# Optimization experiments

Hardware: AMD Instinct MI355X
Metric: run time of the kernel (lower is better)

Reference implementation:

```python
import jax, jax.numpy as jnp
import numpy as np

BN_EPS = 1e-5

def _bn_train(h, gamma, beta):
    # BatchNorm1d in training mode: biased batch stats over the edge (batch) dim
    mean = jnp.mean(h, axis=0)
    var = jnp.var(h, axis=0)
    return (h - mean) * jax.lax.rsqrt(var + BN_EPS) * gamma + beta

def setup_inputs() -> dict:
    key = jax.random.key(0)
    ks = jax.random.split(key, 8)
    N, C, E = 50000, 128, 600000
    x = jax.random.normal(ks[0], (N, C), dtype=jnp.float32)
    edge_index = jax.random.randint(ks[1], (2, E), 0, N, dtype=jnp.int64)
    # Linear params, Kaiming-uniform-ish scale (values don't matter for correctness)
    def lin(k, fan_in, fan_out):
        k1, k2 = jax.random.split(k)
        bound = 1.0 / np.sqrt(fan_in)
        W = jax.random.uniform(k1, (fan_out, fan_in), jnp.float32, -bound, bound)
        b = jax.random.uniform(k2, (fan_out,), jnp.float32, -bound, bound)
        return W, b
    W1, b1 = lin(ks[2], 2 * C, C)
    W2, b2 = lin(ks[3], C, C)
    W3, b3 = lin(ks[4], C, 1)
    g1 = jnp.ones((C,), jnp.float32); be1 = jnp.zeros((C,), jnp.float32)
    g2 = jnp.ones((C,), jnp.float32); be2 = jnp.zeros((C,), jnp.float32)
    return {"x": x, "edge_index": edge_index,
            "W1": W1, "b1": b1, "g1": g1, "be1": be1,
            "W2": W2, "b2": b2, "g2": g2, "be2": be2,
            "W3": W3, "b3": b3}

def reference(x, edge_index, W1, b1, g1, be1, W2, b2, g2, be2, W3, b3):
    # gather endpoint features and concat: [E, 2C]
    ef = jnp.concatenate([x[edge_index[0]], x[edge_index[1]]], axis=1)
    h = jnp.einsum('ec,oc->eo', ef, W1) + b1          # [E, C]
    h = jax.nn.relu(_bn_train(h, g1, be1))
    h = jnp.einsum('ec,oc->eo', h, W2) + b2           # [E, C]
    h = jax.nn.relu(_bn_train(h, g2, be2))
    h = jnp.einsum('ec,oc->eo', h, W3) + b3           # [E, 1]
    return jnp.squeeze(h)                             # [E]
```

## Files before the change

### kernel.cpp

```cpp
#include <hip/hip_runtime.h>
#include <hip/hip_bf16.h>

#define CH 128

constexpr float BN_EPS = 1e-5f;

typedef short bf16x8 __attribute__((ext_vector_type(8)));
typedef float f32x4  __attribute__((ext_vector_type(4)));

__device__ __forceinline__ unsigned cvtpk_bf16(float lo, float hi) {
    unsigned r;
    asm("v_cvt_pk_bf16_f32 %0, %1, %2" : "=v"(r) : "v"(lo), "v"(hi));
    return r;
}
__device__ __forceinline__ float bf2f_lo(unsigned u) { return __uint_as_float(u << 16); }
__device__ __forceinline__ float bf2f_hi(unsigned u) { return __uint_as_float(u & 0xffff0000u); }

__device__ __forceinline__ void lds_barrier() {
    asm volatile("s_waitcnt lgkmcnt(0)\n\ts_barrier" ::: "memory");
}

union BF8 { bf16x8 v; unsigned u[4]; };

__device__ __forceinline__ bf16x8 pack8(float f0, float f1, float f2, float f3,
                                        float f4, float f5, float f6, float f7) {
    BF8 r;
    r.u[0] = cvtpk_bf16(f0, f1);
    r.u[1] = cvtpk_bf16(f2, f3);
    r.u[2] = cvtpk_bf16(f4, f5);
    r.u[3] = cvtpk_bf16(f6, f7);
    return r.v;
}

__global__ __launch_bounds__(512, 4) void node_linear_kernel(
    const float* __restrict__ x, const float* __restrict__ W1,
    unsigned short* __restrict__ u_bf, unsigned short* __restrict__ v_bf, int N)
{
    __shared__ short xs[64 * 128];

    const int t = threadIdx.x;
    const int lane = t & 63;
    const int wv = t >> 6;
    const int l15 = lane & 15;
    const int l4 = lane >> 4;
    const int n0 = blockIdx.x * 64;

    bf16x8 wfrag[2][4];
    #pragma unroll
    for (int ot = 0; ot < 2; ++ot) {
        const int o_ = wv * 32 + ot * 16 + l15;
        const float* wrow = (o_ < 128) ? (W1 + (size_t)o_ * 256)
                                       : (W1 + (size_t)(o_ - 128) * 256 + 128);
        #pragma unroll
        for (int kk = 0; kk < 4; ++kk) {
            float4 a = *(const float4*)(wrow + kk * 32 + l4 * 8);
            float4 b = *(const float4*)(wrow + kk * 32 + l4 * 8 + 4);
            wfrag[ot][kk] = pack8(a.x, a.y, a.z, a.w, b.x, b.y, b.z, b.w);
        }
    }

    const int c16 = t & 15;
    const int cb = c16 * 8;
    const int nsl = t >> 4;
    #pragma unroll
    for (int nn = 0; nn < 2; ++nn) {
        const int n_loc = nsl + nn * 32;
        const int n = n0 + n_loc;
        bf16x8 xv = {0, 0, 0, 0, 0, 0, 0, 0};
        if (n < N) {
            float4 a = *(const float4*)(x + (size_t)n * CH + cb);
            float4 b = *(const float4*)(x + (size_t)n * CH + cb + 4);
            xv = pack8(a.x, a.y, a.z, a.w, b.x, b.y, b.z, b.w);
        }
        *(bf16x8*)(xs + n_loc * 128 + (c16 ^ (n_loc & 7)) * 8) = xv;
    }
    __syncthreads();

    unsigned short* ob = (wv < 4) ? u_bf : v_bf;
    const int chb = (wv & 3) * 32;

    #pragma unroll
    for (int g = 0; g < 4; ++g) {
        const int nrow = g * 16 + l15;
        f32x4 D0 = {0.f, 0.f, 0.f, 0.f};
        f32x4 D1 = {0.f, 0.f, 0.f, 0.f};
        #pragma unroll
        for (int kk = 0; kk < 4; ++kk) {
            bf16x8 a = *(const bf16x8*)(xs + nrow * 128 + ((kk * 4 + l4) ^ (l15 & 7)) * 8);
            D0 = __builtin_amdgcn_mfma_f32_16x16x32_bf16(a, wfrag[0][kk], D0, 0, 0, 0);
            D1 = __builtin_amdgcn_mfma_f32_16x16x32_bf16(a, wfrag[1][kk], D1, 0, 0, 0);
        }
        #pragma unroll
        for (int r = 0; r < 4; ++r) {
            const int n = n0 + g * 16 + l4 * 4 + r;
            if (n < N) {
                unsigned pk = cvtpk_bf16(D0[r], D1[r]);
                ob[(size_t)n * CH + chb + l15]      = (unsigned short)pk;
                ob[(size_t)n * CH + chb + 16 + l15] = (unsigned short)(pk >> 16);
            }
        }
    }
}

__global__ __launch_bounds__(256) void stats1_kernel(
    const unsigned short* __restrict__ u_bf, const unsigned short* __restrict__ v_bf,
    const int* __restrict__ src, const int* __restrict__ dst,
    float* __restrict__ partials, int E)
{
    const int t = threadIdx.x;
    const int c8 = t & 31;
    const int eslot = t >> 5;
    const uint2* u2 = (const uint2*)u_bf;
    const uint2* v2 = (const uint2*)v_bf;

    float rs0=0.f, rs1=0.f, rs2=0.f, rs3=0.f;
    float rq0=0.f, rq1=0.f, rq2=0.f, rq3=0.f;

    const int iters = (E + 15) >> 4;
    for (int it = blockIdx.x; it < iters; it += gridDim.x) {
        const int e0 = it * 16 + eslot;
        const int e1 = e0 + 8;
        if (e0 < E) {
            const int s = src[e0], d = dst[e0];
            const uint2 a = u2[(size_t)s * 32 + c8];
            const uint2 b = v2[(size_t)d * 32 + c8];
            float h;
            h = bf2f_lo(a.x) + bf2f_lo(b.x); rs0 += h; rq0 += h * h;
            h = bf2f_hi(a.x) + bf2f_hi(b.x); rs1 += h; rq1 += h * h;
            h = bf2f_lo(a.y) + bf2f_lo(b.y); rs2 += h; rq2 += h * h;
            h = bf2f_hi(a.y) + bf2f_hi(b.y); rs3 += h; rq3 += h * h;
        }
        if (e1 < E) {
            const int s = src[e1], d = dst[e1];
            const uint2 a = u2[(size_t)s * 32 + c8];
            const uint2 b = v2[(size_t)d * 32 + c8];
            float h;
            h = bf2f_lo(a.x) + bf2f_lo(b.x); rs0 += h; rq0 += h * h;
            h = bf2f_hi(a.x) + bf2f_hi(b.x); rs1 += h; rq1 += h * h;
            h = bf2f_lo(a.y) + bf2f_lo(b.y); rs2 += h; rq2 += h * h;
            h = bf2f_hi(a.y) + bf2f_hi(b.y); rs3 += h; rq3 += h * h;
        }
    }
    __shared__ float red[256];
    red[t] = 0.f;
    __syncthreads();
    const int c = c8 * 4;
    atomicAdd(&red[c + 0], rs0); atomicAdd(&red[c + 1], rs1);
    atomicAdd(&red[c + 2], rs2); atomicAdd(&red[c + 3], rs3);
    atomicAdd(&red[128 + c + 0], rq0); atomicAdd(&red[128 + c + 1], rq1);
    atomicAdd(&red[128 + c + 2], rq2); atomicAdd(&red[128 + c + 3], rq3);
    __syncthreads();
    partials[(size_t)blockIdx.x * 256 + t] = red[t];
}

__global__ __launch_bounds__(1024) void finalize_kernel(
    const float* __restrict__ partials, int nblocks,
    const float* __restrict__ gamma, const float* __restrict__ beta,
    const float* __restrict__ bias,
    float* __restrict__ scale, float* __restrict__ shift, float invE)
{
    __shared__ float accs[1024], accq[1024];
    const int t = threadIdx.x;
    const int ch = t & 127;
    const int sl = t >> 7;
    float s = 0.f, q = 0.f;
    for (int b = sl; b < nblocks; b += 8) {
        s += partials[(size_t)b * 256 + ch];
        q += partials[(size_t)b * 256 + 128 + ch];
    }
    accs[t] = s; accq[t] = q;
    __syncthreads();
    if (t < 128) {
        float st = 0.f, qt = 0.f;
        #pragma unroll
        for (int k = 0; k < 8; ++k) { st += accs[k * 128 + t]; qt += accq[k * 128 + t]; }
        const float m0 = st * invE;
        const float var = fmaxf(qt * invE - m0 * m0, 0.f);
        const float mean = m0 + (bias ? bias[t] : 0.f);
        const float sc = gamma[t] * rsqrtf(var + BN_EPS);
        scale[t] = sc;
        shift[t] = beta[t] - mean * sc;
    }
}

__global__ __launch_bounds__(512, 4) void layer2_kernel(
    const unsigned short* __restrict__ u_bf, const unsigned short* __restrict__ v_bf,
    const int* __restrict__ src, const int* __restrict__ dst,
    const float* __restrict__ b1,
    const float* __restrict__ scale1, const float* __restrict__ shift1,
    const float* __restrict__ W2, const float* __restrict__ b2,
    uint2* __restrict__ h2raw, float* __restrict__ partials, int E)
{
    __shared__ short ybuf[2][64 * 128];
    __shared__ float red[256];

    const int t = threadIdx.x;
    const int lane = t & 63;
    const int wv = t >> 6;
    const int p = wv & 3;
    const int h = wv >> 2;
    const int l15 = lane & 15;
    const int l4  = lane >> 4;

    bf16x8 wfrag[2][4];
    #pragma unroll
    for (int ot = 0; ot < 2; ++ot) {
        const int o = p * 32 + ot * 16 + l15;
        #pragma unroll
        for (int kk = 0; kk < 4; ++kk) {
            const float* wp = W2 + (size_t)o * CH + kk * 32 + l4 * 8;
            float4 a = *(const float4*)wp;
            float4 bq = *(const float4*)(wp + 4);
            wfrag[ot][kk] = pack8(a.x, a.y, a.z, a.w, bq.x, bq.y, bq.z, bq.w);
        }
    }
    float b2r[2][4];
    #pragma unroll
    for (int ot = 0; ot < 2; ++ot)
        #pragma unroll
        for (int r = 0; r < 4; ++r)
            b2r[ot][r] = b2[p * 32 + ot * 16 + l4 * 4 + r];

    const int c16 = t & 15;
    const int cb = c16 * 8;
    const int ebase = t >> 4;
    const float4 sca = *(const float4*)(scale1 + cb);
    const float4 scb = *(const float4*)(scale1 + cb + 4);
    const float4 sha = *(const float4*)(shift1 + cb);
    const float4 shb = *(const float4*)(shift1 + cb + 4);
    const float4 b1a = *(const float4*)(b1 + cb);
    const float4 b1b = *(const float4*)(b1 + cb + 4);
    float4 bsa, bsb;
    bsa.x = b1a.x*sca.x + sha.x; bsa.y = b1a.y*sca.y + sha.y;
    bsa.z = b1a.z*sca.z + sha.z; bsa.w = b1a.w*sca.w + sha.w;
    bsb.x = b1b.x*scb.x + shb.x; bsb.y = b1b.y*scb.y + shb.y;
    bsb.z = b1b.z*scb.z + shb.z; bsb.w = b1b.w*scb.w + shb.w;

    float rs[2][4] = {{0.f,0.f,0.f,0.f},{0.f,0.f,0.f,0.f}};
    float rq[2][4] = {{0.f,0.f,0.f,0.f},{0.f,0.f,0.f,0.f}};

    const int ntiles = (E + 63) >> 6;
    const int tstep = gridDim.x;

    uint4 ua0, va0, ua1, va1;
    int tile = blockIdx.x;
    if (tile < ntiles) {
        const int eA = tile * 64 + ebase;
        const int eB = eA + 32;
        const int cA = eA < E ? eA : E - 1;
        const int cB = eB < E ? eB : E - 1;
        const int sA = src[cA], dA = dst[cA];
        const int sB = src[cB], dB = dst[cB];
        ua0 = *(const uint4*)(u_bf + (size_t)sA * CH + cb);
        va0 = *(const uint4*)(v_bf + (size_t)dA * CH + cb);
        ua1 = *(const uint4*)(u_bf + (size_t)sB * CH + cb);
        va1 = *(const uint4*)(v_bf + (size_t)dB * CH + cb);
    }

    int cur = 0;
    for (; tile < ntiles; tile += tstep) {
        {
            const int e = tile * 64 + ebase;
            bf16x8 y8 = {0, 0, 0, 0, 0, 0, 0, 0};
            if (e < E) {
                const float f0 = bf2f_lo(ua0.x) + bf2f_lo(va0.x);
                const float f1 = bf2f_hi(ua0.x) + bf2f_hi(va0.x);
                const float f2 = bf2f_lo(ua0.y) + bf2f_lo(va0.y);
                const float f3 = bf2f_hi(ua0.y) + bf2f_hi(va0.y);
                const float f4 = bf2f_lo(ua0.z) + bf2f_lo(va0.z);
                const float f5 = bf2f_hi(ua0.z) + bf2f_hi(va0.z);
                const float f6 = bf2f_lo(ua0.w) + bf2f_lo(va0.w);
                const float f7 = bf2f_hi(ua0.w) + bf2f_hi(va0.w);
                y8 = pack8(fmaxf(f0 * sca.x + bsa.x, 0.f),
                           fmaxf(f1 * sca.y + bsa.y, 0.f),
                           fmaxf(f2 * sca.z + bsa.z, 0.f),
                           fmaxf(f3 * sca.w + bsa.w, 0.f),
                           fmaxf(f4 * scb.x + bsb.x, 0.f),
                           fmaxf(f5 * scb.y + bsb.y, 0.f),
                           fmaxf(f6 * scb.z + bsb.z, 0.f),
                           fmaxf(f7 * scb.w + bsb.w, 0.f));
            }
            *(bf16x8*)(ybuf[cur] + ebase * 128 + (c16 ^ (ebase & 7)) * 8) = y8;
        }
        {
            const int e_loc = ebase + 32;
            const int e = tile * 64 + e_loc;
            bf16x8 y8 = {0, 0, 0, 0, 0, 0, 0, 0};
            if (e < E) {
                const float f0 = bf2f_lo(ua1.x) + bf2f_lo(va1.x);
                const float f1 = bf2f_hi(ua1.x) + bf2f_hi(va1.x);
                const float f2 = bf2f_lo(ua1.y) + bf2f_lo(va1.y);
                const float f3 = bf2f_hi(ua1.y) + bf2f_hi(va1.y);
                const float f4 = bf2f_lo(ua1.z) + bf2f_lo(va1.z);
                const float f5 = bf2f_hi(ua1.z) + bf2f_hi(va1.z);
                const float f6 = bf2f_lo(ua1.w) + bf2f_lo(va1.w);
                const float f7 = bf2f_hi(ua1.w) + bf2f_hi(va1.w);
                y8 = pack8(fmaxf(f0 * sca.x + bsa.x, 0.f),
                           fmaxf(f1 * sca.y + bsa.y, 0.f),
                           fmaxf(f2 * sca.z + bsa.z, 0.f),
                           fmaxf(f3 * sca.w + bsa.w, 0.f),
                           fmaxf(f4 * scb.x + bsb.x, 0.f),
                           fmaxf(f5 * scb.y + bsb.y, 0.f),
                           fmaxf(f6 * scb.z + bsb.z, 0.f),
                           fmaxf(f7 * scb.w + bsb.w, 0.f));
            }
            *(bf16x8*)(ybuf[cur] + e_loc * 128 + (c16 ^ (ebase & 7)) * 8) = y8;
        }

        const int ntile = tile + tstep;
        if (ntile < ntiles) {
            const int eA = ntile * 64 + ebase;
            const int eB = eA + 32;
            const int cA = eA < E ? eA : E - 1;
            const int cB = eB < E ? eB : E - 1;
            const int sA = src[cA], dA = dst[cA];
            const int sB = src[cB], dB = dst[cB];
            ua0 = *(const uint4*)(u_bf + (size_t)sA * CH + cb);
            va0 = *(const uint4*)(v_bf + (size_t)dA * CH + cb);
            ua1 = *(const uint4*)(u_bf + (size_t)sB * CH + cb);
            va1 = *(const uint4*)(v_bf + (size_t)dB * CH + cb);
        }

        lds_barrier();

        #pragma unroll
        for (int g2 = 0; g2 < 2; ++g2) {
            const int g = h * 2 + g2;
            const int erow = g * 16 + l15;
            f32x4 D0 = {0.f, 0.f, 0.f, 0.f};
            f32x4 D1 = {0.f, 0.f, 0.f, 0.f};
            #pragma unroll
            for (int kk = 0; kk < 4; ++kk) {
                bf16x8 yf = *(const bf16x8*)(ybuf[cur] + erow * 128 + ((kk * 4 + l4) ^ (l15 & 7)) * 8);
                D0 = __builtin_amdgcn_mfma_f32_16x16x32_bf16(wfrag[0][kk], yf, D0, 0, 0, 0);
                D1 = __builtin_amdgcn_mfma_f32_16x16x32_bf16(wfrag[1][kk], yf, D1, 0, 0, 0);
            }
            const int gblk = tile * 4 + g;
            const bool ev = ((size_t)gblk * 16 + l15) < (size_t)E;
            {
                const float a0 = D0[0] + b2r[0][0], a1 = D0[1] + b2r[0][1];
                const float a2 = D0[2] + b2r[0][2], a3 = D0[3] + b2r[0][3];
                rs[0][0] += ev ? a0 : 0.f; rq[0][0] += ev ? a0 * a0 : 0.f;
                rs[0][1] += ev ? a1 : 0.f; rq[0][1] += ev ? a1 * a1 : 0.f;
                rs[0][2] += ev ? a2 : 0.f; rq[0][2] += ev ? a2 * a2 : 0.f;
                rs[0][3] += ev ? a3 : 0.f; rq[0][3] += ev ? a3 * a3 : 0.f;
                h2raw[((size_t)gblk * 8 + p * 2 + 0) * 64 + lane] =
                    make_uint2(cvtpk_bf16(a0, a1), cvtpk_bf16(a2, a3));
            }
            {
                const float c0 = D1[0] + b2r[1][0], c1 = D1[1] + b2r[1][1];
                const float c2 = D1[2] + b2r[1][2], c3 = D1[3] + b2r[1][3];
                rs[1][0] += ev ? c0 : 0.f; rq[1][0] += ev ? c0 * c0 : 0.f;
                rs[1][1] += ev ? c1 : 0.f; rq[1][1] += ev ? c1 * c1 : 0.f;
                rs[1][2] += ev ? c2 : 0.f; rq[1][2] += ev ? c2 * c2 : 0.f;
                rs[1][3] += ev ? c3 : 0.f; rq[1][3] += ev ? c3 * c3 : 0.f;
                h2raw[((size_t)gblk * 8 + p * 2 + 1) * 64 + lane] =
                    make_uint2(cvtpk_bf16(c0, c1), cvtpk_bf16(c2, c3));
            }
        }
        cur ^= 1;
    }

    __syncthreads();
    if (t < 256) red[t] = 0.f;
    __syncthreads();
    #pragma unroll
    for (int ot = 0; ot < 2; ++ot) {
        #pragma unroll
        for (int r = 0; r < 4; ++r) {
            float a = rs[ot][r], b = rq[ot][r];
            #pragma unroll
            for (int m = 1; m <= 8; m <<= 1) {
                a += __shfl_xor(a, m, 64);
                b += __shfl_xor(b, m, 64);
            }
            if (l15 == 0) {
                const int ch = p * 32 + ot * 16 + l4 * 4 + r;
                atomicAdd(&red[ch], a);
                atomicAdd(&red[128 + ch], b);
            }
        }
    }
    __syncthreads();
    if (t < 256) partials[(size_t)blockIdx.x * 256 + t] = red[t];
}

__global__ __launch_bounds__(256) void output_kernel(
    const uint2* __restrict__ h2raw,
    const float* __restrict__ scale2, const float* __restrict__ shift2,
    const float* __restrict__ W3, const float* __restrict__ b3,
    float* __restrict__ out, int E)
{
    __shared__ float sc_s[128], sh_s[128], w3_s[128];
    const int t = threadIdx.x;
    if (t < 128) { sc_s[t] = scale2[t]; sh_s[t] = shift2[t]; w3_s[t] = W3[t]; }
    __syncthreads();
    const int wv = t >> 6;
    const int lane = t & 63;
    const int l15 = lane & 15;
    const int l4 = lane >> 4;
    const float bias = b3[0];
    const int ngrp = (E + 15) >> 4;
    const int gstep = gridDim.x * 4;
    for (int g0 = blockIdx.x * 4 + wv; g0 < ngrp; g0 += 2 * gstep) {
        const int g1 = g0 + gstep;
        float acc0 = 0.f, acc1 = 0.f;
        #pragma unroll
        for (int w = 0; w < 8; ++w) {
            const uint2 raw = h2raw[((size_t)g0 * 8 + w) * 64 + lane];
            const int o = w * 16 + l4 * 4;
            const float4 sc = *(const float4*)(sc_s + o);
            const float4 sh = *(const float4*)(sh_s + o);
            const float4 w3 = *(const float4*)(w3_s + o);
            acc0 += fmaxf(bf2f_lo(raw.x) * sc.x + sh.x, 0.f) * w3.x;
            acc0 += fmaxf(bf2f_hi(raw.x) * sc.y + sh.y, 0.f) * w3.y;
            acc0 += fmaxf(bf2f_lo(raw.y) * sc.z + sh.z, 0.f) * w3.z;
            acc0 += fmaxf(bf2f_hi(raw.y) * sc.w + sh.w, 0.f) * w3.w;
        }
        if (g1 < ngrp) {
            #pragma unroll
            for (int w = 0; w < 8; ++w) {
                const uint2 raw = h2raw[((size_t)g1 * 8 + w) * 64 + lane];
                const int o = w * 16 + l4 * 4;
                const float4 sc = *(const float4*)(sc_s + o);
                const float4 sh = *(const float4*)(sh_s + o);
                const float4 w3 = *(const float4*)(w3_s + o);
                acc1 += fmaxf(bf2f_lo(raw.x) * sc.x + sh.x, 0.f) * w3.x;
                acc1 += fmaxf(bf2f_hi(raw.x) * sc.y + sh.y, 0.f) * w3.y;
                acc1 += fmaxf(bf2f_lo(raw.y) * sc.z + sh.z, 0.f) * w3.z;
                acc1 += fmaxf(bf2f_hi(raw.y) * sc.w + sh.w, 0.f) * w3.w;
            }
        }
        acc0 += __shfl_xor(acc0, 16, 64);
        acc0 += __shfl_xor(acc0, 32, 64);
        acc1 += __shfl_xor(acc1, 16, 64);
        acc1 += __shfl_xor(acc1, 32, 64);
        if (l4 == 0) {
            const int e0 = g0 * 16 + l15;
            if (e0 < E) out[e0] = acc0 + bias;
            if (g1 < ngrp) {
                const int e1 = g1 * 16 + l15;
                if (e1 < E) out[e1] = acc1 + bias;
            }
        }
    }
}

extern "C" void kernel_launch(void* const* d_in, const int* in_sizes, int n_in,
                              void* d_out, int out_size, void* d_ws, size_t ws_size,
                              hipStream_t stream)
{
    const float* x   = (const float*)d_in[0];
    const int*   ei  = (const int*)d_in[1];
    const float* W1  = (const float*)d_in[2];
    const float* b1  = (const float*)d_in[3];
    const float* g1  = (const float*)d_in[4];
    const float* be1 = (const float*)d_in[5];
    const float* W2  = (const float*)d_in[6];
    const float* b2  = (const float*)d_in[7];
    const float* g2  = (const float*)d_in[8];
    const float* be2 = (const float*)d_in[9];
    const float* W3  = (const float*)d_in[10];
    const float* b3  = (const float*)d_in[11];

    const int N = in_sizes[0] / CH;
    const int E = out_size;
    const int* src = ei;
    const int* dst = ei + E;

    const int S1_BLOCKS = 2048;
    const int S2_BLOCKS = 1024;
    const size_t ngblk = (size_t)((E + 63) >> 6) * 4;

    unsigned short* u_bf = (unsigned short*)d_ws;
    unsigned short* v_bf = u_bf + (size_t)N * CH;
    uint2* h2raw = (uint2*)(v_bf + (size_t)N * CH);
    float* part1 = (float*)(h2raw + ngblk * 8 * 64);
    float* part2 = part1 + (size_t)S1_BLOCKS * 256;
    float* scale1 = part2 + (size_t)S2_BLOCKS * 256;
    float* shift1 = scale1 + CH;
    float* scale2 = shift1 + CH;
    float* shift2 = scale2 + CH;
    float* out = (float*)d_out;

    node_linear_kernel<<<(N + 63) / 64, 512, 0, stream>>>(x, W1, u_bf, v_bf, N);
    stats1_kernel<<<S1_BLOCKS, 256, 0, stream>>>(u_bf, v_bf, src, dst, part1, E);
    finalize_kernel<<<1, 1024, 0, stream>>>(part1, S1_BLOCKS, g1, be1, b1,
                                            scale1, shift1, 1.0f / (float)E);
    layer2_kernel<<<S2_BLOCKS, 512, 0, stream>>>(u_bf, v_bf, src, dst, b1, scale1, shift1,
                                                 W2, b2, h2raw, part2, E);
    finalize_kernel<<<1, 1024, 0, stream>>>(part2, S2_BLOCKS, g2, be2, nullptr,
                                            scale2, shift2, 1.0f / (float)E);
    output_kernel<<<2048, 256, 0, stream>>>(h2raw, scale2, shift2, W3, b3, out, E);
}
```

Measured before the change: 307.9 us.

## Prefetch next tile's gathers in stats1 with 16-byte loads and shuffle reduction

Rewrites the layer-1 statistics kernel so each thread gathers 8 bf16 channels with one 16-byte load per endpoint instead of 4 channels with 8-byte loads. The gathers for the next 64-edge tile are issued before the current tile is accumulated, which software-pipelines the latency of the random gathers. Blocks grow to 512 threads and the grid is halved. The final reduction uses wave shuffles before the LDS atomics, which cuts atomic contention. The cost is more registers per thread and fewer blocks.

Result: faster. 260.3 us (median of 2 runs) (-15.5%).

```diff
diff --git a/kernel.cpp b/kernel.cpp
--- a/kernel.cpp
+++ b/kernel.cpp
@@ -102,55 +102,92 @@
     }
 }
 
-__global__ __launch_bounds__(256) void stats1_kernel(
+__global__ __launch_bounds__(512, 4) void stats1_kernel(
     const unsigned short* __restrict__ u_bf, const unsigned short* __restrict__ v_bf,
     const int* __restrict__ src, const int* __restrict__ dst,
     float* __restrict__ partials, int E)
 {
     const int t = threadIdx.x;
-    const int c8 = t & 31;
-    const int eslot = t >> 5;
-    const uint2* u2 = (const uint2*)u_bf;
-    const uint2* v2 = (const uint2*)v_bf;
-
-    float rs0=0.f, rs1=0.f, rs2=0.f, rs3=0.f;
-    float rq0=0.f, rq1=0.f, rq2=0.f, rq3=0.f;
-
-    const int iters = (E + 15) >> 4;
-    for (int it = blockIdx.x; it < iters; it += gridDim.x) {
-        const int e0 = it * 16 + eslot;
-        const int e1 = e0 + 8;
+    const int lane = t & 63;
+    const int c16 = t & 15;
+    const int cb = c16 * 8;
+    const int ebase = t >> 4;
+
+    float rs[8] = {0.f,0.f,0.f,0.f,0.f,0.f,0.f,0.f};
+    float rq[8] = {0.f,0.f,0.f,0.f,0.f,0.f,0.f,0.f};
+
+    const int ntiles = (E + 63) >> 6;
+    const int tstep = gridDim.x;
+
+    uint4 ua0, va0, ua1, va1;
+    int tile = blockIdx.x;
+    if (tile < ntiles) {
+        const int eA = tile * 64 + ebase;
+        const int eB = eA + 32;
+        const int cA = eA < E ? eA : E - 1;
+        const int cB = eB < E ? eB : E - 1;
+        ua0 = *(const uint4*)(u_bf + (size_t)src[cA] * CH + cb);
+        va0 = *(const uint4*)(v_bf + (size_t)dst[cA] * CH + cb);
+        ua1 = *(const uint4*)(u_bf + (size_t)src[cB] * CH + cb);
+        va1 = *(const uint4*)(v_bf + (size_t)dst[cB] * CH + cb);
+    }
+
+    for (; tile < ntiles; tile += tstep) {
+        const uint4 cua0 = ua0, cva0 = va0, cua1 = ua1, cva1 = va1;
+        const int e0 = tile * 64 + ebase;
+        const int e1 = e0 + 32;
+
+        const int ntile = tile + tstep;
+        if (ntile < ntiles) {
+            const int eA = ntile * 64 + ebase;
+            const int eB = eA + 32;
+            const int cA = eA < E ? eA : E - 1;
+            const int cB = eB < E ? eB : E - 1;
+            ua0 = *(const uint4*)(u_bf + (size_t)src[cA] * CH + cb);
+            va0 = *(const uint4*)(v_bf + (size_t)dst[cA] * CH + cb);
+            ua1 = *(const uint4*)(u_bf + (size_t)src[cB] * CH + cb);
+            va1 = *(const uint4*)(v_bf + (size_t)dst[cB] * CH + cb);
+        }
+
         if (e0 < E) {
-            const int s = src[e0], d = dst[e0];
-            const uint2 a = u2[(size_t)s * 32 + c8];
-            const uint2 b = v2[(size_t)d * 32 + c8];
             float h;
-            h = bf2f_lo(a.x) + bf2f_lo(b.x); rs0 += h; rq0 += h * h;
-            h = bf2f_hi(a.x) + bf2f_hi(b.x); rs1 += h; rq1 += h * h;
-            h = bf2f_lo(a.y) + bf2f_lo(b.y); rs2 += h; rq2 += h * h;
-            h = bf2f_hi(a.y) + bf2f_hi(b.y); rs3 += h; rq3 += h * h;
+            h = bf2f_lo(cua0.x) + bf2f_lo(cva0.x); rs[0] += h; rq[0] += h * h;
+            h = bf2f_hi(cua0.x) + bf2f_hi(cva0.x); rs[1] += h; rq[1] += h * h;
+            h = bf2f_lo(cua0.y) + bf2f_lo(cva0.y); rs[2] += h; rq[2] += h * h;
+            h = bf2f_hi(cua0.y) + bf2f_hi(cva0.y); rs[3] += h; rq[3] += h * h;
+            h = bf2f_lo(cua0.z) + bf2f_lo(cva0.z); rs[4] += h; rq[4] += h * h;
+            h = bf2f_hi(cua0.z) + bf2f_hi(cva0.z); rs[5] += h; rq[5] += h * h;
+            h = bf2f_lo(cua0.w) + bf2f_lo(cva0.w); rs[6] += h; rq[6] += h * h;
+            h = bf2f_hi(cua0.w) + bf2f_hi(cva0.w); rs[7] += h; rq[7] += h * h;
         }
         if (e1 < E) {
-            const int s = src[e1], d = dst[e1];
-            const uint2 a = u2[(size_t)s * 32 + c8];
-            const uint2 b = v2[(size_t)d * 32 + c8];
             float h;
-            h = bf2f_lo(a.x) + bf2f_lo(b.x); rs0 += h; rq0 += h * h;
-            h = bf2f_hi(a.x) + bf2f_hi(b.x); rs1 += h; rq1 += h * h;
-            h = bf2f_lo(a.y) + bf2f_lo(b.y); rs2 += h; rq2 += h * h;
-            h = bf2f_hi(a.y) + bf2f_hi(b.y); rs3 += h; rq3 += h * h;
-        }
-    }
+            h = bf2f_lo(cua1.x) + bf2f_lo(cva1.x); rs[0] += h; rq[0] += h * h;
+            h = bf2f_hi(cua1.x) + bf2f_hi(cva1.x); rs[1] += h; rq[1] += h * h;
+            h = bf2f_lo(cua1.y) + bf2f_lo(cva1.y); rs[2] += h; rq[2] += h * h;
+            h = bf2f_hi(cua1.y) + bf2f_hi(cva1.y); rs[3] += h; rq[3] += h * h;
+            h = bf2f_lo(cua1.z) + bf2f_lo(cva1.z); rs[4] += h; rq[4] += h * h;
+            h = bf2f_hi(cua1.z) + bf2f_hi(cva1.z); rs[5] += h; rq[5] += h * h;
+            h = bf2f_lo(cua1.w) + bf2f_lo(cva1.w); rs[6] += h; rq[6] += h * h;
+            h = bf2f_hi(cua1.w) + bf2f_hi(cva1.w); rs[7] += h; rq[7] += h * h;
+        }
+    }
+
     __shared__ float red[256];
-    red[t] = 0.f;
-    __syncthreads();
-    const int c = c8 * 4;
-    atomicAdd(&red[c + 0], rs0); atomicAdd(&red[c + 1], rs1);
-    atomicAdd(&red[c + 2], rs2); atomicAdd(&red[c + 3], rs3);
-    atomicAdd(&red[128 + c + 0], rq0); atomicAdd(&red[128 + c + 1], rq1);
-    atomicAdd(&red[128 + c + 2], rq2); atomicAdd(&red[128 + c + 3], rq3);
-    __syncthreads();
-    partials[(size_t)blockIdx.x * 256 + t] = red[t];
+    if (t < 256) red[t] = 0.f;
+    __syncthreads();
+    #pragma unroll
+    for (int k = 0; k < 8; ++k) {
+        float a = rs[k], b = rq[k];
+        a += __shfl_xor(a, 16, 64); a += __shfl_xor(a, 32, 64);
+        b += __shfl_xor(b, 16, 64); b += __shfl_xor(b, 32, 64);
+        if ((lane & 48) == 0) {
+            atomicAdd(&red[cb + k], a);
+            atomicAdd(&red[128 + cb + k], b);
+        }
+    }
+    __syncthreads();
+    if (t < 256) partials[(size_t)blockIdx.x * 256 + t] = red[t];
 }
 
 __global__ __launch_bounds__(1024) void finalize_kernel(
@@ -468,7 +505,7 @@
     const int* src = ei;
     const int* dst = ei + E;
 
-    const int S1_BLOCKS = 2048;
+    const int S1_BLOCKS = 1024;
     const int S2_BLOCKS = 1024;
     const size_t ngblk = (size_t)((E + 63) >> 6) * 4;
 
@@ -484,7 +521,7 @@
     float* out = (float*)d_out;
 
     node_linear_kernel<<<(N + 63) / 64, 512, 0, stream>>>(x, W1, u_bf, v_bf, N);
-    stats1_kernel<<<S1_BLOCKS, 256, 0, stream>>>(u_bf, v_bf, src, dst, part1, E);
+    stats1_kernel<<<S1_BLOCKS, 512, 0, stream>>>(u_bf, v_bf, src, dst, part1, E);
     finalize_kernel<<<1, 1024, 0, stream>>>(part1, S1_BLOCKS, g1, be1, b1,
                                             scale1, shift1, 1.0f / (float)E);
     layer2_kernel<<<S2_BLOCKS, 512, 0, stream>>>(u_bf, v_bf, src, dst, b1, scale1, shift1,
```
